# Kernel tuning notes

Hardware: AMD Instinct MI355X
Metric: run time of the kernel (lower is better)

Reference implementation:

```python
import jax, jax.numpy as jnp
import numpy as np

B_, S, D = 4, 4096, 2048   # batch, seq, d_model
OUT = 2048
E, R = 8, 16               # num_experts, lora rank
ALPHA = 32.0
SCALING = ALPHA / R


def setup_inputs() -> dict:
    key = jax.random.key(0)
    ks = jax.random.split(key, 6)
    x = jax.random.normal(ks[0], (B_, S, D), dtype=jnp.float32)
    W_base = jax.random.normal(ks[1], (OUT, D), dtype=jnp.float32) * (D ** -0.5)
    b_base = jax.random.normal(ks[2], (OUT,), dtype=jnp.float32) * 0.01
    router_W = jax.random.normal(ks[3], (E, D), dtype=jnp.float32) * (D ** -0.5)
    A = jax.random.normal(ks[4], (E, R, D), dtype=jnp.float32) * (D ** -0.5)   # lora_A weights [E, r, in]
    Bw = jax.random.normal(ks[5], (E, OUT, R), dtype=jnp.float32) * 0.02       # lora_B weights [E, out, r]
    return {"x": x, "W_base": W_base, "b_base": b_base, "router_W": router_W, "A": A, "Bw": Bw}


def reference(x, W_base, b_base, router_W, A, Bw):
    # frozen base linear
    base_out = jnp.einsum('bsd,od->bso', x, W_base) + b_base
    # router on detached input, top-1 expert
    logits = jnp.einsum('bsd,ed->bse', jax.lax.stop_gradient(x), router_W)
    routing_probs = jax.nn.softmax(logits, axis=-1)
    expert_idx = jnp.argmax(routing_probs, axis=-1)                 # [B,S]
    onehot = jax.nn.one_hot(expert_idx, E, dtype=x.dtype)           # [B,S,E]
    # LoRA down-proj for all experts (cheap: r=16), mask to selected expert
    h = jnp.einsum('bsd,erd->bser', x, A)                           # [B,S,E,R]
    h = h * onehot[..., None]
    # up-proj, combine over experts (only selected one is nonzero)
    delta = jnp.einsum('bser,eor->bso', h, Bw)                      # [B,S,OUT]
    return base_out + delta * SCALING
```

## Files before the change

### kernel.cpp

```cpp
#include <hip/hip_runtime.h>

#define D_    2048
#define OUT_  2048
#define E_    8
#define R_    16
#define KX    2176
#define M_    16384
#define SCALING_F 2.0f

typedef unsigned short ushort_t;
typedef unsigned short ushort8 __attribute__((ext_vector_type(8)));
typedef __bf16 bf16x8 __attribute__((ext_vector_type(8)));
typedef float f32x4 __attribute__((ext_vector_type(4)));

__device__ __forceinline__ ushort_t f2bf(float f) {
  unsigned u = __float_as_uint(f);
  u += 0x7FFFu + ((u >> 16) & 1u);
  return (ushort_t)(u >> 16);
}

#define GLOAD16(gp, lp)                                                        \
  __builtin_amdgcn_global_load_lds(                                            \
      (const __attribute__((address_space(1))) void*)(gp),                     \
      (__attribute__((address_space(3))) void*)(lp), 16, 0, 0)

__global__ __launch_bounds__(256) void wprep_kernel(
    const float* __restrict__ W, const float* __restrict__ Bw,
    ushort_t* __restrict__ wext)
{
  const int o = blockIdx.x;
  const int t = threadIdx.x;
  const float* wr = W + (size_t)o * D_ + t * 8;
  float4 v0 = *(const float4*)wr;
  float4 v1 = *(const float4*)(wr + 4);
  ushort8 wb;
  wb[0] = f2bf(v0.x); wb[1] = f2bf(v0.y); wb[2] = f2bf(v0.z); wb[3] = f2bf(v0.w);
  wb[4] = f2bf(v1.x); wb[5] = f2bf(v1.y); wb[6] = f2bf(v1.z); wb[7] = f2bf(v1.w);
  *(ushort8*)(wext + (size_t)o * KX + t * 8) = wb;
  if (t < E_ * R_) {
    const int e = t >> 4, r = t & 15;
    wext[(size_t)o * KX + D_ + t] = f2bf(Bw[((size_t)e * OUT_ + o) * R_ + r]);
  }
}

__global__ __launch_bounds__(256) void aprep_kernel(
    const float* __restrict__ A, ushort_t* __restrict__ aext)
{
  const size_t i = ((size_t)blockIdx.x * 256 + threadIdx.x) * 8;
  float4 v0 = *(const float4*)(A + i);
  float4 v1 = *(const float4*)(A + i + 4);
  ushort8 b;
  b[0] = f2bf(v0.x); b[1] = f2bf(v0.y); b[2] = f2bf(v0.z); b[3] = f2bf(v0.w);
  b[4] = f2bf(v1.x); b[5] = f2bf(v1.y); b[6] = f2bf(v1.z); b[7] = f2bf(v1.w);
  *(ushort8*)(aext + i) = b;
}

__global__ __launch_bounds__(256) void router_kernel(
    const float* __restrict__ x, const float* __restrict__ rW,
    ushort_t* __restrict__ xext, int* __restrict__ eidx)
{
  const int t = threadIdx.x, lane = t & 63, wid = t >> 6;
  const int m0 = (blockIdx.x * 4 + wid) * 4;

  float acc[4][E_];
  #pragma unroll
  for (int k = 0; k < 4; ++k)
    #pragma unroll
    for (int e = 0; e < E_; ++e) acc[k][e] = 0.f;

  #pragma unroll
  for (int j = 0; j < 8; ++j) {
    const int col = j * 256 + lane * 4;
    float4 w[E_];
    #pragma unroll
    for (int e = 0; e < E_; ++e)
      w[e] = *(const float4*)(rW + (size_t)e * D_ + col);
    #pragma unroll
    for (int k = 0; k < 4; ++k) {
      float4 xv = *(const float4*)(x + (size_t)(m0 + k) * D_ + col);
      ushort4 xb;
      xb.x = f2bf(xv.x); xb.y = f2bf(xv.y); xb.z = f2bf(xv.z); xb.w = f2bf(xv.w);
      *(ushort4*)(xext + (size_t)(m0 + k) * KX + col) = xb;
      #pragma unroll
      for (int e = 0; e < E_; ++e)
        acc[k][e] += xv.x * w[e].x + xv.y * w[e].y + xv.z * w[e].z + xv.w * w[e].w;
    }
  }

  #pragma unroll
  for (int k = 0; k < 4; ++k) {
    double s0 = acc[k][0], s1 = acc[k][1], s2 = acc[k][2], s3 = acc[k][3];
    double s4 = acc[k][4], s5 = acc[k][5], s6 = acc[k][6], s7 = acc[k][7];
    #pragma unroll
    for (int off = 32; off; off >>= 1) {
      s0 += __shfl_xor(s0, off, 64); s1 += __shfl_xor(s1, off, 64);
      s2 += __shfl_xor(s2, off, 64); s3 += __shfl_xor(s3, off, 64);
      s4 += __shfl_xor(s4, off, 64); s5 += __shfl_xor(s5, off, 64);
      s6 += __shfl_xor(s6, off, 64); s7 += __shfl_xor(s7, off, 64);
    }
    int bi = 0; double best = s0;
    if (s1 > best) { best = s1; bi = 1; }
    if (s2 > best) { best = s2; bi = 2; }
    if (s3 > best) { best = s3; bi = 3; }
    if (s4 > best) { best = s4; bi = 4; }
    if (s5 > best) { best = s5; bi = 5; }
    if (s6 > best) { best = s6; bi = 6; }
    if (s7 > best) { best = s7; bi = 7; }
    if (lane == 0) eidx[m0 + k] = bi;
  }
}

#define HG_NKT (D_ / 64)

__global__ __launch_bounds__(256) void hgemm_kernel(
    const ushort_t* __restrict__ Xg,
    const ushort_t* __restrict__ Ae,
    const int* __restrict__ eidx,
    ushort_t* __restrict__ xext)
{
  __shared__ __attribute__((aligned(16))) char lds[40960];

  const int t = threadIdx.x;
  const int lane = t & 63, w = t >> 6;
  const int wr = w >> 1, wc = w & 1;
  const int lr = lane & 15, lg = lane >> 4;
  const int koff = (lr & 7) << 4;

  const int bm = blockIdx.x;
  const size_t row0 = (size_t)bm * 32;

  const int sg_row = t >> 3;
  const int sg_slotx = (t & 7) ^ ((t >> 3) & 7);

  auto stage = [&](int TT) {
    char* dst = lds + (TT & 1) * 20480;
    GLOAD16(Xg + (row0 + sg_row) * KX + TT * 64 + sg_slotx * 8, dst + t * 16);
    #pragma unroll
    for (int g = 0; g < 4; ++g) {
      const int r = g * 32 + sg_row;
      GLOAD16(Ae + (size_t)r * D_ + TT * 64 + sg_slotx * 8,
              dst + 4096 + g * 4096 + t * 16);
    }
  };

  f32x4 acc[4] = {};

  stage(0);
  asm volatile("s_waitcnt vmcnt(0)" ::: "memory");
  __builtin_amdgcn_s_barrier();

  for (int T = 0; T < HG_NKT; ++T) {
    if (T + 1 < HG_NKT) stage(T + 1);
    char* Ab = lds + (T & 1) * 20480;
    char* Bb = Ab + 4096;
    bf16x8 af[2], bfr[4][2];
    #pragma unroll
    for (int kk = 0; kk < 2; ++kk)
      af[kk] = *(const bf16x8*)(Ab + (wr * 16 + lr) * 128 + ((kk * 64 + lg * 16) ^ koff));
    #pragma unroll
    for (int nj = 0; nj < 4; ++nj) {
      const int R = wc * 64 + nj * 16 + lr;
      #pragma unroll
      for (int kk = 0; kk < 2; ++kk)
        bfr[nj][kk] = *(const bf16x8*)(Bb + R * 128 + ((kk * 64 + lg * 16) ^ koff));
    }
    #pragma unroll
    for (int nj = 0; nj < 4; ++nj)
      #pragma unroll
      for (int kk = 0; kk < 2; ++kk)
        acc[nj] = __builtin_amdgcn_mfma_f32_16x16x32_bf16(af[kk], bfr[nj][kk], acc[nj], 0, 0, 0);
    asm volatile("s_waitcnt vmcnt(0)" ::: "memory");
    __builtin_amdgcn_s_barrier();
  }

  int er[4];
  #pragma unroll
  for (int rr = 0; rr < 4; ++rr)
    er[rr] = eidx[row0 + wr * 16 + lg * 4 + rr];
  #pragma unroll
  for (int nj = 0; nj < 4; ++nj) {
    const int col = wc * 64 + nj * 16 + lr;
    const int ecol = wc * 4 + nj;
    #pragma unroll
    for (int rr = 0; rr < 4; ++rr) {
      const size_t row = row0 + wr * 16 + lg * 4 + rr;
      ushort_t v = (er[rr] == ecol) ? f2bf(acc[nj][rr] * SCALING_F) : (ushort_t)0;
      xext[row * KX + D_ + col] = v;
    }
  }
}

#define NKT (KX / 64)
#define NSTG (NKT * 4)

__global__ __launch_bounds__(512, 2) void gemm_kernel(
    const ushort_t* __restrict__ Ag,
    const ushort_t* __restrict__ Bg,
    const float* __restrict__ bias,
    float* __restrict__ C)
{
  __shared__ __attribute__((aligned(16))) char lds[131072];

  const int t = threadIdx.x;
  const int lane = t & 63, w = t >> 6;
  const int wm = w >> 2, wn = w & 3;
  const int lr = lane & 15, lg = lane >> 4;
  const int koff = (lr & 7) << 4;

  const int swz = (blockIdx.x & 7) * 64 + (blockIdx.x >> 3);
  const int bm = swz >> 3, bn = swz & 7;

  const int sg_row = t >> 3;
  const int sg_slotx = (t & 7) ^ ((t >> 3) & 7);
  const size_t aRow0 = (size_t)bm * 256;
  const size_t bRow0 = (size_t)bn * 256;

  auto stage = [&](int s) {
    if (s >= NSTG) return;
    const int TT = s >> 2, j = s & 3;
    const int isB = j >> 1, half = j & 1;
    const ushort_t* src = isB ? Bg : Ag;
    const size_t gr0 = (isB ? bRow0 : aRow0) + half * 128;
    char* dst = lds + (TT & 1) * 65536 + isB * 32768 + half * 16384;
    #pragma unroll
    for (int g = 0; g < 2; ++g) {
      const int r = g * 64 + sg_row;
      GLOAD16(src + (gr0 + r) * KX + TT * 64 + sg_slotx * 8,
              dst + g * 8192 + t * 16);
    }
  };

  f32x4 acc[8][4] = {};
  bf16x8 bq[4][2];

  stage(0); stage(1); stage(2); stage(3); stage(4);
  asm volatile("s_waitcnt vmcnt(2)" ::: "memory");
  __builtin_amdgcn_s_barrier();

  #pragma unroll 2
  for (int T = 0; T < NKT; ++T) {
    char* Ab = lds + (T & 1) * 65536;
    char* Bb = Ab + 32768;
    #pragma unroll
    for (int q = 0; q < 4; ++q) {
      bf16x8 aq[2][2];
      if (q == 0) {
        #pragma unroll
        for (int nj = 0; nj < 4; ++nj) {
          const int R = wn * 64 + nj * 16 + lr;
          #pragma unroll
          for (int kk = 0; kk < 2; ++kk)
            bq[nj][kk] = *(const bf16x8*)(Bb + R * 128 + ((kk * 64 + lg * 16) ^ koff));
        }
      }
      #pragma unroll
      for (int i = 0; i < 2; ++i) {
        const int R = wm * 128 + (q * 2 + i) * 16 + lr;
        #pragma unroll
        for (int kk = 0; kk < 2; ++kk)
          aq[i][kk] = *(const bf16x8*)(Ab + R * 128 + ((kk * 64 + lg * 16) ^ koff));
      }
      stage(4 * T + 5 + q);
      if (q == 0) asm volatile("s_waitcnt lgkmcnt(8)" ::: "memory");
      __builtin_amdgcn_s_barrier();
      asm volatile("s_waitcnt lgkmcnt(0)" ::: "memory");
      __builtin_amdgcn_s_setprio(1);
      #pragma unroll
      for (int i = 0; i < 2; ++i)
        #pragma unroll
        for (int nj = 0; nj < 4; ++nj)
          #pragma unroll
          for (int kk = 0; kk < 2; ++kk)
            acc[q * 2 + i][nj] = __builtin_amdgcn_mfma_f32_16x16x32_bf16(
                aq[i][kk], bq[nj][kk], acc[q * 2 + i][nj], 0, 0, 0);
      __builtin_amdgcn_s_setprio(0);
      if (q == 3) {
        if (T >= NKT - 2) asm volatile("s_waitcnt vmcnt(0)" ::: "memory");
        else              asm volatile("s_waitcnt vmcnt(2)" ::: "memory");
      }
      __builtin_amdgcn_s_barrier();
    }
  }

  #pragma unroll
  for (int nj = 0; nj < 4; ++nj) {
    const int col = bn * 256 + wn * 64 + nj * 16 + lr;
    const float bv = bias[col];
    #pragma unroll
    for (int mi = 0; mi < 8; ++mi) {
      const int row0 = bm * 256 + wm * 128 + mi * 16 + lg * 4;
      #pragma unroll
      for (int rr = 0; rr < 4; ++rr)
        C[(size_t)(row0 + rr) * OUT_ + col] = acc[mi][nj][rr] + bv;
    }
  }
}

extern "C" void kernel_launch(void* const* d_in, const int* in_sizes, int n_in,
                              void* d_out, int out_size, void* d_ws, size_t ws_size,
                              hipStream_t stream) {
  const float* x  = (const float*)d_in[0];
  const float* Wb = (const float*)d_in[1];
  const float* bb = (const float*)d_in[2];
  const float* rW = (const float*)d_in[3];
  const float* A  = (const float*)d_in[4];
  const float* Bw = (const float*)d_in[5];
  float* out = (float*)d_out;

  ushort_t* xext = (ushort_t*)d_ws;
  ushort_t* wext = (ushort_t*)((char*)d_ws + (size_t)M_ * KX * 2);
  int* eidx = (int*)((char*)d_ws + (size_t)M_ * KX * 2 + (size_t)OUT_ * KX * 2);
  ushort_t* aext = (ushort_t*)((char*)eidx + M_ * sizeof(int));

  wprep_kernel<<<OUT_, 256, 0, stream>>>(Wb, Bw, wext);
  aprep_kernel<<<(E_ * R_ * D_) / (256 * 8), 256, 0, stream>>>(A, aext);
  router_kernel<<<M_ / 16, 256, 0, stream>>>(x, rW, xext, eidx);
  hgemm_kernel<<<M_ / 32, 256, 0, stream>>>(xext, aext, eidx, xext);
  gemm_kernel<<<(M_ / 256) * (OUT_ / 256), 512, 0, stream>>>(xext, wext, bb, out);
}
```

Before: 267.9 us.

## Fuse weight prep kernels, move x bf16 conversion into hgemm, reorder gemm prefetch

Merges the W and A fp32-to-bf16 prep kernels into one launch. The router no longer writes bf16 x; hgemm now reads fp32 x directly, converts it into LDS and writes the bf16 copy to xext, which removes one pass of bf16 x traffic. The router reduction does its first shuffle stages in float and only the later ones in double, cutting double-shuffle cost, at a possible small risk to exact argmax ties. The main GEMM prefetch order is changed so B tiles are issued further ahead, with deeper vmcnt waits.

```diff
diff --git a/kernel.cpp b/kernel.cpp
--- a/kernel.cpp
+++ b/kernel.cpp
@@ -24,40 +24,40 @@
       (const __attribute__((address_space(1))) void*)(gp),                     \
       (__attribute__((address_space(3))) void*)(lp), 16, 0, 0)
 
-__global__ __launch_bounds__(256) void wprep_kernel(
+__global__ __launch_bounds__(256) void wprep_all_kernel(
     const float* __restrict__ W, const float* __restrict__ Bw,
-    ushort_t* __restrict__ wext)
+    const float* __restrict__ A,
+    ushort_t* __restrict__ wext, ushort_t* __restrict__ aext)
 {
-  const int o = blockIdx.x;
+  const int bid = blockIdx.x;
   const int t = threadIdx.x;
-  const float* wr = W + (size_t)o * D_ + t * 8;
-  float4 v0 = *(const float4*)wr;
-  float4 v1 = *(const float4*)(wr + 4);
-  ushort8 wb;
-  wb[0] = f2bf(v0.x); wb[1] = f2bf(v0.y); wb[2] = f2bf(v0.z); wb[3] = f2bf(v0.w);
-  wb[4] = f2bf(v1.x); wb[5] = f2bf(v1.y); wb[6] = f2bf(v1.z); wb[7] = f2bf(v1.w);
-  *(ushort8*)(wext + (size_t)o * KX + t * 8) = wb;
-  if (t < E_ * R_) {
-    const int e = t >> 4, r = t & 15;
-    wext[(size_t)o * KX + D_ + t] = f2bf(Bw[((size_t)e * OUT_ + o) * R_ + r]);
-  }
-}
-
-__global__ __launch_bounds__(256) void aprep_kernel(
-    const float* __restrict__ A, ushort_t* __restrict__ aext)
-{
-  const size_t i = ((size_t)blockIdx.x * 256 + threadIdx.x) * 8;
-  float4 v0 = *(const float4*)(A + i);
-  float4 v1 = *(const float4*)(A + i + 4);
-  ushort8 b;
-  b[0] = f2bf(v0.x); b[1] = f2bf(v0.y); b[2] = f2bf(v0.z); b[3] = f2bf(v0.w);
-  b[4] = f2bf(v1.x); b[5] = f2bf(v1.y); b[6] = f2bf(v1.z); b[7] = f2bf(v1.w);
-  *(ushort8*)(aext + i) = b;
+  if (bid < OUT_) {
+    const int o = bid;
+    const float* wr = W + (size_t)o * D_ + t * 8;
+    float4 v0 = *(const float4*)wr;
+    float4 v1 = *(const float4*)(wr + 4);
+    ushort8 wb;
+    wb[0] = f2bf(v0.x); wb[1] = f2bf(v0.y); wb[2] = f2bf(v0.z); wb[3] = f2bf(v0.w);
+    wb[4] = f2bf(v1.x); wb[5] = f2bf(v1.y); wb[6] = f2bf(v1.z); wb[7] = f2bf(v1.w);
+    *(ushort8*)(wext + (size_t)o * KX + t * 8) = wb;
+    if (t < E_ * R_) {
+      const int e = t >> 4, r = t & 15;
+      wext[(size_t)o * KX + D_ + t] = f2bf(Bw[((size_t)e * OUT_ + o) * R_ + r]);
+    }
+  } else {
+    const size_t i = ((size_t)(bid - OUT_) * 256 + t) * 8;
+    float4 v0 = *(const float4*)(A + i);
+    float4 v1 = *(const float4*)(A + i + 4);
+    ushort8 b;
+    b[0] = f2bf(v0.x); b[1] = f2bf(v0.y); b[2] = f2bf(v0.z); b[3] = f2bf(v0.w);
+    b[4] = f2bf(v1.x); b[5] = f2bf(v1.y); b[6] = f2bf(v1.z); b[7] = f2bf(v1.w);
+    *(ushort8*)(aext + i) = b;
+  }
 }
 
 __global__ __launch_bounds__(256) void router_kernel(
     const float* __restrict__ x, const float* __restrict__ rW,
-    ushort_t* __restrict__ xext, int* __restrict__ eidx)
+    int* __restrict__ eidx)
 {
   const int t = threadIdx.x, lane = t & 63, wid = t >> 6;
   const int m0 = (blockIdx.x * 4 + wid) * 4;
@@ -78,9 +78,6 @@
     #pragma unroll
     for (int k = 0; k < 4; ++k) {
       float4 xv = *(const float4*)(x + (size_t)(m0 + k) * D_ + col);
-      ushort4 xb;
-      xb.x = f2bf(xv.x); xb.y = f2bf(xv.y); xb.z = f2bf(xv.z); xb.w = f2bf(xv.w);
-      *(ushort4*)(xext + (size_t)(m0 + k) * KX + col) = xb;
       #pragma unroll
       for (int e = 0; e < E_; ++e)
         acc[k][e] += xv.x * w[e].x + xv.y * w[e].y + xv.z * w[e].z + xv.w * w[e].w;
@@ -89,23 +86,24 @@
 
   #pragma unroll
   for (int k = 0; k < 4; ++k) {
-    double s0 = acc[k][0], s1 = acc[k][1], s2 = acc[k][2], s3 = acc[k][3];
-    double s4 = acc[k][4], s5 = acc[k][5], s6 = acc[k][6], s7 = acc[k][7];
-    #pragma unroll
-    for (int off = 32; off; off >>= 1) {
-      s0 += __shfl_xor(s0, off, 64); s1 += __shfl_xor(s1, off, 64);
-      s2 += __shfl_xor(s2, off, 64); s3 += __shfl_xor(s3, off, 64);
-      s4 += __shfl_xor(s4, off, 64); s5 += __shfl_xor(s5, off, 64);
-      s6 += __shfl_xor(s6, off, 64); s7 += __shfl_xor(s7, off, 64);
-    }
-    int bi = 0; double best = s0;
-    if (s1 > best) { best = s1; bi = 1; }
-    if (s2 > best) { best = s2; bi = 2; }
-    if (s3 > best) { best = s3; bi = 3; }
-    if (s4 > best) { best = s4; bi = 4; }
-    if (s5 > best) { best = s5; bi = 5; }
-    if (s6 > best) { best = s6; bi = 6; }
-    if (s7 > best) { best = s7; bi = 7; }
+    float r[E_];
+    #pragma unroll
+    for (int e = 0; e < E_; ++e) r[e] = acc[k][e];
+    #pragma unroll
+    for (int off = 1; off <= 4; off <<= 1)
+      #pragma unroll
+      for (int e = 0; e < E_; ++e) r[e] += __shfl_xor(r[e], off, 64);
+    double s[E_];
+    #pragma unroll
+    for (int e = 0; e < E_; ++e) s[e] = (double)r[e];
+    #pragma unroll
+    for (int off = 8; off <= 32; off <<= 1)
+      #pragma unroll
+      for (int e = 0; e < E_; ++e) s[e] += __shfl_xor(s[e], off, 64);
+    int bi = 0; double best = s[0];
+    #pragma unroll
+    for (int e = 1; e < E_; ++e)
+      if (s[e] > best) { best = s[e]; bi = e; }
     if (lane == 0) eidx[m0 + k] = bi;
   }
 }
@@ -113,7 +111,7 @@
 #define HG_NKT (D_ / 64)
 
 __global__ __launch_bounds__(256) void hgemm_kernel(
-    const ushort_t* __restrict__ Xg,
+    const float* __restrict__ x,
     const ushort_t* __restrict__ Ae,
     const int* __restrict__ eidx,
     ushort_t* __restrict__ xext)
@@ -130,47 +128,67 @@
   const size_t row0 = (size_t)bm * 32;
 
   const int sg_row = t >> 3;
-  const int sg_slotx = (t & 7) ^ ((t >> 3) & 7);
-
-  auto stage = [&](int TT) {
-    char* dst = lds + (TT & 1) * 20480;
-    GLOAD16(Xg + (row0 + sg_row) * KX + TT * 64 + sg_slotx * 8, dst + t * 16);
+  const int sg_c = t & 7;
+  const int sg_slotx = sg_c ^ (sg_row & 7);
+
+  auto stageA = [&](int TT) {
+    char* dst = lds + (TT & 1) * 20480 + 4096;
     #pragma unroll
     for (int g = 0; g < 4; ++g) {
       const int r = g * 32 + sg_row;
       GLOAD16(Ae + (size_t)r * D_ + TT * 64 + sg_slotx * 8,
-              dst + 4096 + g * 4096 + t * 16);
+              dst + g * 4096 + t * 16);
     }
   };
+  auto putX = [&](int TT, const float4& a, const float4& b) {
+    ushort8 xb;
+    xb[0] = f2bf(a.x); xb[1] = f2bf(a.y); xb[2] = f2bf(a.z); xb[3] = f2bf(a.w);
+    xb[4] = f2bf(b.x); xb[5] = f2bf(b.y); xb[6] = f2bf(b.z); xb[7] = f2bf(b.w);
+    char* Xb = lds + (TT & 1) * 20480;
+    *(ushort8*)(Xb + sg_row * 128 + sg_slotx * 16) = xb;
+    *(ushort8*)(xext + (row0 + sg_row) * KX + TT * 64 + sg_c * 8) = xb;
+  };
 
   f32x4 acc[4] = {};
 
-  stage(0);
-  asm volatile("s_waitcnt vmcnt(0)" ::: "memory");
-  __builtin_amdgcn_s_barrier();
+  {
+    const float* xp = x + (row0 + sg_row) * D_ + sg_c * 8;
+    float4 a = *(const float4*)xp;
+    float4 b = *(const float4*)(xp + 4);
+    stageA(0);
+    putX(0, a, b);
+  }
+  __syncthreads();
 
   for (int T = 0; T < HG_NKT; ++T) {
-    if (T + 1 < HG_NKT) stage(T + 1);
-    char* Ab = lds + (T & 1) * 20480;
-    char* Bb = Ab + 4096;
+    float4 na, nb;
+    const bool more = (T + 1 < HG_NKT);
+    if (more) {
+      const float* xp = x + (row0 + sg_row) * D_ + (T + 1) * 64 + sg_c * 8;
+      na = *(const float4*)xp;
+      nb = *(const float4*)(xp + 4);
+      stageA(T + 1);
+    }
+    char* Xb = lds + (T & 1) * 20480;
+    char* Ab = Xb + 4096;
     bf16x8 af[2], bfr[4][2];
     #pragma unroll
     for (int kk = 0; kk < 2; ++kk)
-      af[kk] = *(const bf16x8*)(Ab + (wr * 16 + lr) * 128 + ((kk * 64 + lg * 16) ^ koff));
+      af[kk] = *(const bf16x8*)(Xb + (wr * 16 + lr) * 128 + ((kk * 64 + lg * 16) ^ koff));
     #pragma unroll
     for (int nj = 0; nj < 4; ++nj) {
       const int R = wc * 64 + nj * 16 + lr;
       #pragma unroll
       for (int kk = 0; kk < 2; ++kk)
-        bfr[nj][kk] = *(const bf16x8*)(Bb + R * 128 + ((kk * 64 + lg * 16) ^ koff));
+        bfr[nj][kk] = *(const bf16x8*)(Ab + R * 128 + ((kk * 64 + lg * 16) ^ koff));
     }
     #pragma unroll
     for (int nj = 0; nj < 4; ++nj)
       #pragma unroll
       for (int kk = 0; kk < 2; ++kk)
         acc[nj] = __builtin_amdgcn_mfma_f32_16x16x32_bf16(af[kk], bfr[nj][kk], acc[nj], 0, 0, 0);
-    asm volatile("s_waitcnt vmcnt(0)" ::: "memory");
-    __builtin_amdgcn_s_barrier();
+    if (more) putX(T + 1, na, nb);
+    __syncthreads();
   }
 
   int er[4];
@@ -233,8 +251,9 @@
   f32x4 acc[8][4] = {};
   bf16x8 bq[4][2];
 
-  stage(0); stage(1); stage(2); stage(3); stage(4);
-  asm volatile("s_waitcnt vmcnt(2)" ::: "memory");
+  stage(0); stage(1); stage(2); stage(3);
+  stage(6); stage(7);
+  asm volatile("s_waitcnt vmcnt(4)" ::: "memory");
   __builtin_amdgcn_s_barrier();
 
   #pragma unroll 2
@@ -260,7 +279,7 @@
         for (int kk = 0; kk < 2; ++kk)
           aq[i][kk] = *(const bf16x8*)(Ab + R * 128 + ((kk * 64 + lg * 16) ^ koff));
       }
-      stage(4 * T + 5 + q);
+      stage(q < 2 ? 4 * (T + 1) + q : 4 * (T + 2) + q);
       if (q == 0) asm volatile("s_waitcnt lgkmcnt(8)" ::: "memory");
       __builtin_amdgcn_s_barrier();
       asm volatile("s_waitcnt lgkmcnt(0)" ::: "memory");
@@ -276,7 +295,7 @@
       __builtin_amdgcn_s_setprio(0);
       if (q == 3) {
         if (T >= NKT - 2) asm volatile("s_waitcnt vmcnt(0)" ::: "memory");
-        else              asm volatile("s_waitcnt vmcnt(2)" ::: "memory");
+        else              asm volatile("s_waitcnt vmcnt(4)" ::: "memory");
       }
       __builtin_amdgcn_s_barrier();
     }
@@ -312,9 +331,8 @@
   int* eidx = (int*)((char*)d_ws + (size_t)M_ * KX * 2 + (size_t)OUT_ * KX * 2);
   ushort_t* aext = (ushort_t*)((char*)eidx + M_ * sizeof(int));
 
-  wprep_kernel<<<OUT_, 256, 0, stream>>>(Wb, Bw, wext);
-  aprep_kernel<<<(E_ * R_ * D_) / (256 * 8), 256, 0, stream>>>(A, aext);
-  router_kernel<<<M_ / 16, 256, 0, stream>>>(x, rW, xext, eidx);
-  hgemm_kernel<<<M_ / 32, 256, 0, stream>>>(xext, aext, eidx, xext);
+  wprep_all_kernel<<<OUT_ + (E_ * R_ * D_) / (256 * 8), 256, 0, stream>>>(Wb, Bw, A, wext, aext);
+  router_kernel<<<M_ / 16, 256, 0, stream>>>(x, rW, eidx);
+  hgemm_kernel<<<M_ / 32, 256, 0, stream>>>(x, aext, eidx, xext);
   gemm_kernel<<<(M_ / 256) * (OUT_ / 256), 512, 0, stream>>>(xext, wext, bb, out);
 }
```

Result: faster. 245.5 us (-8.4%).
